# Kernel optimization log

Measured on AMD Instinct MI355X. Metric: run time of the kernel, lower is better.

## Reference

```python
import jax, jax.numpy as jnp
import numpy as np
from jax.scipy.special import gammaln

INTERVAL_STEPS = (1, -1, -3, 3, 4, -4)
MARGIN = 0.5


def _build_transition(S):
    # T[f, t, i] = 1 if t == f + interval_steps[i], else 0 (within support)
    T = np.zeros((S, S, len(INTERVAL_STEPS)), dtype=np.float32)
    for i, s in enumerate(INTERVAL_STEPS):
        if s > 0:
            f = np.arange(0, S - s)
        else:
            f = np.arange(-s, S)
        T[f, f + s, i] = 1.0
    return jnp.asarray(T)


def _forward(data, log_weights):
    n_data, C = data.shape
    S = int(np.ceil((2 * MARGIN + 1) * C))              # n_dist_support = 256
    center = int(np.round((MARGIN + 0.5) * C))           # reference_center = 128
    down = -min(min(INTERVAL_STEPS), 0)
    up = max(max(INTERVAL_STEPS), 0)
    n_iters = int(np.ceil(max(center / down, (S - center) / up))) + 1  # 33
    T = _build_transition(S)

    # Poisson-weighted Markov diffusion
    w = jnp.exp(log_weights)
    rate = w.sum(axis=1)                                 # [d]
    p = w / rate[:, None]                                # [d, i] interval step probs
    log_rate = jnp.log(rate)
    run0 = jnp.zeros((n_data, S), data.dtype).at[:, center].set(1.0)
    acc0 = jnp.zeros((n_data, S), data.dtype)

    def diff_step(carry, n):
        acc, run = carry
        step_prob = jnp.exp(n * log_rate - rate - gammaln(n + 1.0))  # Poisson pmf(n)
        acc = acc + step_prob[:, None] * run
        # einsum('fti,di,df->dt') done as two controlled contractions
        tmp = jnp.einsum('fti,df->dti', T, run)          # [d, t, i]
        run = jnp.einsum('dti,di->dt', tmp, p)           # [d, t]
        return (acc, run), None

    (acc, _), _ = jax.lax.scan(diff_step, (acc0, run0),
                               jnp.arange(n_iters, dtype=data.dtype))
    icd = acc / acc.sum(axis=1, keepdims=True)           # [d, S]

    # match distributions: min over shifts of DKL(data || normalized slice)
    n_shifts = S - C + 1
    pz = jnp.isclose(data, 0.0)
    safe_p = jnp.where(pz, 1.0, data)
    plogp = jnp.where(pz, 0.0, data * jnp.log(safe_p))   # [d, C]

    def match_step(carry, shift):
        best_loss, best_dist = carry
        d = jax.lax.dynamic_slice_in_dim(icd, shift, C, axis=1)
        d = d / d.sum(axis=1, keepdims=True)
        logq = jnp.log(jnp.maximum(d, 1e-38))            # guard fp32 underflow at edges
        loss = (plogp - jnp.where(pz, 0.0, data * logq)).sum(axis=1)
        cond = loss < best_loss
        return (jnp.where(cond, loss, best_loss),
                jnp.where(cond[:, None], d, best_dist)), None

    init = (jnp.full((n_data,), jnp.inf, data.dtype), jnp.zeros_like(data))
    (matched_loss, matched_dist), _ = jax.lax.scan(match_step, init, jnp.arange(n_shifts))
    return matched_loss


def setup_inputs() -> dict:
    key = jax.random.key(0)
    k1, k2 = jax.random.split(key)
    u = jax.random.uniform(k1, (4096, 128), jnp.float32)
    data = u / u.sum(axis=1, keepdims=True)              # rows are distributions
    # small weights -> Poisson rates ~6, so cum prob is allclose(1) before iter 33,
    # matching the original module's break-at-effective_min_iterations behavior
    log_weights = 0.1 * jax.random.normal(k2, (4096, 6), jnp.float32)
    return {"data": data, "log_weights": log_weights}


def reference(data, log_weights):
    return _forward(data, log_weights)
```

## Files before the change

kernel.cpp:

```cpp
#include <hip/hip_runtime.h>
#include <math.h>

#define NC      128
#define NSTATE  256
#define NITERS  33
#define NSTEPS  6
#define RPB     4
#define CL2     (-126.22347f)
#define LN2     (0.6931471805599453f)

__global__ __launch_bounds__(256)
void tonal_diffusion_kernel(const float* __restrict__ data,
                            const float* __restrict__ logw,
                            float* __restrict__ out, int n_rows)
{
    const int wid  = threadIdx.x >> 6;
    const int lane = threadIdx.x & 63;
    const int row  = blockIdx.x * RPB + wid;
    if (row >= n_rows) return;

    __shared__ float licd_s[RPB][NSTATE];
    __shared__ float P_s   [RPB][NSTATE];
    __shared__ float dsh_s [RPB][NC];
    float* __restrict__ licd = licd_s[wid];
    float* __restrict__ P    = P_s[wid];
    float* __restrict__ dsh  = dsh_s[wid];

    float rate, p0, p1, p2, p3, p4, p5;
    {
        const float* lw = logw + row * NSTEPS;
        p0 = expf(lw[0]); p1 = expf(lw[1]); p2 = expf(lw[2]);
        p3 = expf(lw[3]); p4 = expf(lw[4]); p5 = expf(lw[5]);
        rate = ((p0 + p1) + (p2 + p3)) + (p4 + p5);
        const float inv = 1.0f / rate;
        p0 *= inv; p1 *= inv; p2 *= inv; p3 *= inv; p4 *= inv; p5 *= inv;
    }

    float plogp;
    {
        const float2 dv = *(const float2*)(data + row * NC + 2 * lane);
        const float d0 = (dv.x > 1e-8f) ? dv.x : 0.f;
        const float d1 = (dv.y > 1e-8f) ? dv.y : 0.f;
        *(float2*)(dsh + 2 * lane) = make_float2(d0, d1);
        float pl = 0.f;
        if (d0 > 0.f) pl += d0 * logf(d0);
        if (d1 > 0.f) pl += d1 * logf(d1);
        #pragma unroll
        for (int off = 1; off < 64; off <<= 1) pl += __shfl_xor(pl, off, 64);
        plogp = pl;
    }

    float r0 = 0.f, r1 = 0.f, r2 = 0.f, r3 = 0.f;
    if (lane == 32) r0 = 1.0f;
    float a0 = 0.f, a1 = 0.f, a2 = 0.f, a3 = 0.f;
    float sp = expf(-rate);
    const float mL = (lane == 0)  ? 0.f : 1.f;
    const float mR = (lane == 63) ? 0.f : 1.f;
    #pragma unroll
    for (int n = 0; n < NITERS; ++n) {
        a0 += sp * r0; a1 += sp * r1; a2 += sp * r2; a3 += sp * r3;
        const float L0 = __shfl_up(r0, 1, 64) * mL;
        const float L1 = __shfl_up(r1, 1, 64) * mL;
        const float L2 = __shfl_up(r2, 1, 64) * mL;
        const float L3 = __shfl_up(r3, 1, 64) * mL;
        const float R0 = __shfl_down(r0, 1, 64) * mR;
        const float R1 = __shfl_down(r1, 1, 64) * mR;
        const float R2 = __shfl_down(r2, 1, 64) * mR;
        const float R3 = __shfl_down(r3, 1, 64) * mR;
        const float n0 = p0*L3 + p1*r1 + p2*r3 + p3*L1 + p4*L0 + p5*R0;
        const float n1 = p0*r0 + p1*r2 + p2*R0 + p3*L2 + p4*L1 + p5*R1;
        const float n2 = p0*r1 + p1*r3 + p2*R1 + p3*L3 + p4*L2 + p5*R2;
        const float n3 = p0*r2 + p1*R0 + p2*R2 + p3*r0 + p4*L3 + p5*R3;
        r0 = n0; r1 = n1; r2 = n2; r3 = n3;
        sp = sp * rate * (1.0f / (float)(n + 1));
    }

    *(float4*)(licd + 4 * lane) = make_float4(log2f(a0), log2f(a1), log2f(a2), log2f(a3));

    const float s0 = a0, s1 = s0 + a1, s2 = s1 + a2, s3 = s2 + a3;
    float t = s3;
    #pragma unroll
    for (int off = 1; off < 64; off <<= 1) {
        const float u = __shfl_up(t, off, 64);
        if (lane >= off) t += u;
    }
    const float base = t - s3;
    *(float4*)(P + 4 * lane) = make_float4(base + s0, base + s1, base + s2, base + s3);

    const int sA = lane, sB = lane + 64;
    const float zA = log2f(P[sA + 127] - (sA ? P[sA - 1] : 0.f));
    const float zB = log2f(P[sB + 127] - P[sB - 1]);
    float accA = 0.f, accB = 0.f;
    const float* lc = licd + lane;
    #pragma unroll 8
    for (int idx = 0; idx < 64; ++idx)
        accA += dsh[idx] * fmaxf(lc[idx] - zA, CL2);
    #pragma unroll 8
    for (int idx = 64; idx < 128; ++idx) {
        const float v = lc[idx];
        accA += dsh[idx]      * fmaxf(v - zA, CL2);
        accB += dsh[idx - 64] * fmaxf(v - zB, CL2);
    }
    #pragma unroll 8
    for (int idx = 128; idx < 192; ++idx)
        accB += dsh[idx - 64] * fmaxf(lc[idx] - zB, CL2);
    float best = fminf(plogp - LN2 * accA, plogp - LN2 * accB);

    {
        const float z = log2f(P[255] - P[127]);
        float part = dsh[2 * lane]     * fmaxf(licd[128 + 2 * lane] - z, CL2)
                   + dsh[2 * lane + 1] * fmaxf(licd[129 + 2 * lane] - z, CL2);
        #pragma unroll
        for (int off = 1; off < 64; off <<= 1) part += __shfl_xor(part, off, 64);
        best = fminf(best, plogp - LN2 * part);
    }

    #pragma unroll
    for (int off = 1; off < 64; off <<= 1) best = fminf(best, __shfl_xor(best, off, 64));
    if (lane == 0) out[row] = best;
}

extern "C" void kernel_launch(void* const* d_in, const int* in_sizes, int n_in,
                              void* d_out, int out_size, void* d_ws, size_t ws_size,
                              hipStream_t stream)
{
    const float* data = (const float*)d_in[0];
    const float* logw = (const float*)d_in[1];
    float* out = (float*)d_out;
    const int n_rows = in_sizes[0] / NC;
    const int blocks = (n_rows + RPB - 1) / RPB;
    tonal_diffusion_kernel<<<blocks, 256, 0, stream>>>(data, logw, out, n_rows);
}
```

Baseline: 77.79 us.

## Use DPP lane shifts and phase-replicated LDS layout for vectorized shift scan

Replaces ds_bpermute-based shuffles in the diffusion loop with DPP wave shift-by-one (bound_ctrl zero-fills edges, removing mask multiplies). Stores four phase-shifted copies of log-icd in LDS so each lane can read aligned float4 vectors in the shift-matching loop, and reads data from global memory with a wave-uniform row index (scalar loads) instead of staging it in LDS. It trades 4x LDS footprint for fewer LDS instructions and relies on DPP wave_shr/wave_shl being supported on this target. The near-zero clamp on data is also dropped in the accumulation loops.

Result: faster. 75.27 us (-3.2%).

```diff
diff --git a/kernel.cpp b/kernel.cpp
--- a/kernel.cpp
+++ b/kernel.cpp
@@ -9,6 +9,18 @@
 #define CL2     (-126.22347f)
 #define LN2     (0.6931471805599453f)
 
+#define DPP_WAVE_SHL1 0x130
+#define DPP_WAVE_SHR1 0x138
+
+__device__ __forceinline__ float dpp_shr1(float x) {
+    return __int_as_float(__builtin_amdgcn_update_dpp(
+        0, __float_as_int(x), DPP_WAVE_SHR1, 0xf, 0xf, true));
+}
+__device__ __forceinline__ float dpp_shl1(float x) {
+    return __int_as_float(__builtin_amdgcn_update_dpp(
+        0, __float_as_int(x), DPP_WAVE_SHL1, 0xf, 0xf, true));
+}
+
 __global__ __launch_bounds__(256)
 void tonal_diffusion_kernel(const float* __restrict__ data,
                             const float* __restrict__ logw,
@@ -18,17 +30,18 @@
     const int lane = threadIdx.x & 63;
     const int row  = blockIdx.x * RPB + wid;
     if (row >= n_rows) return;
+    const int urow = __builtin_amdgcn_readfirstlane(row);
 
-    __shared__ float licd_s[RPB][NSTATE];
-    __shared__ float P_s   [RPB][NSTATE];
-    __shared__ float dsh_s [RPB][NC];
-    float* __restrict__ licd = licd_s[wid];
-    float* __restrict__ P    = P_s[wid];
-    float* __restrict__ dsh  = dsh_s[wid];
+    __shared__ __align__(16) float licdR_s[RPB][4][NSTATE];
+    __shared__ __align__(16) float P_s    [RPB][NSTATE];
+    float (* __restrict__ licdR)[NSTATE] = licdR_s[wid];
+    float * __restrict__ P               = P_s[wid];
+
+    const float* __restrict__ drow = data + (size_t)urow * NC;
 
     float rate, p0, p1, p2, p3, p4, p5;
     {
-        const float* lw = logw + row * NSTEPS;
+        const float* lw = logw + urow * NSTEPS;
         p0 = expf(lw[0]); p1 = expf(lw[1]); p2 = expf(lw[2]);
         p3 = expf(lw[3]); p4 = expf(lw[4]); p5 = expf(lw[5]);
         rate = ((p0 + p1) + (p2 + p3)) + (p4 + p5);
@@ -36,15 +49,12 @@
         p0 *= inv; p1 *= inv; p2 *= inv; p3 *= inv; p4 *= inv; p5 *= inv;
     }
 
+    const float2 dl = *(const float2*)(drow + 2 * lane);
     float plogp;
     {
-        const float2 dv = *(const float2*)(data + row * NC + 2 * lane);
-        const float d0 = (dv.x > 1e-8f) ? dv.x : 0.f;
-        const float d1 = (dv.y > 1e-8f) ? dv.y : 0.f;
-        *(float2*)(dsh + 2 * lane) = make_float2(d0, d1);
         float pl = 0.f;
-        if (d0 > 0.f) pl += d0 * logf(d0);
-        if (d1 > 0.f) pl += d1 * logf(d1);
+        if (dl.x > 1e-8f) pl += dl.x * logf(dl.x);
+        if (dl.y > 1e-8f) pl += dl.y * logf(dl.y);
         #pragma unroll
         for (int off = 1; off < 64; off <<= 1) pl += __shfl_xor(pl, off, 64);
         plogp = pl;
@@ -54,19 +64,13 @@
     if (lane == 32) r0 = 1.0f;
     float a0 = 0.f, a1 = 0.f, a2 = 0.f, a3 = 0.f;
     float sp = expf(-rate);
-    const float mL = (lane == 0)  ? 0.f : 1.f;
-    const float mR = (lane == 63) ? 0.f : 1.f;
     #pragma unroll
     for (int n = 0; n < NITERS; ++n) {
         a0 += sp * r0; a1 += sp * r1; a2 += sp * r2; a3 += sp * r3;
-        const float L0 = __shfl_up(r0, 1, 64) * mL;
-        const float L1 = __shfl_up(r1, 1, 64) * mL;
-        const float L2 = __shfl_up(r2, 1, 64) * mL;
-        const float L3 = __shfl_up(r3, 1, 64) * mL;
-        const float R0 = __shfl_down(r0, 1, 64) * mR;
-        const float R1 = __shfl_down(r1, 1, 64) * mR;
-        const float R2 = __shfl_down(r2, 1, 64) * mR;
-        const float R3 = __shfl_down(r3, 1, 64) * mR;
+        const float L0 = dpp_shr1(r0), L1 = dpp_shr1(r1),
+                    L2 = dpp_shr1(r2), L3 = dpp_shr1(r3);
+        const float R0 = dpp_shl1(r0), R1 = dpp_shl1(r1),
+                    R2 = dpp_shl1(r2), R3 = dpp_shl1(r3);
         const float n0 = p0*L3 + p1*r1 + p2*r3 + p3*L1 + p4*L0 + p5*R0;
         const float n1 = p0*r0 + p1*r2 + p2*R0 + p3*L2 + p4*L1 + p5*R1;
         const float n2 = p0*r1 + p1*r3 + p2*R1 + p3*L3 + p4*L2 + p5*R2;
@@ -75,41 +79,69 @@
         sp = sp * rate * (1.0f / (float)(n + 1));
     }
 
-    *(float4*)(licd + 4 * lane) = make_float4(log2f(a0), log2f(a1), log2f(a2), log2f(a3));
+    {
+        const float l0 = log2f(a0), l1 = log2f(a1), l2 = log2f(a2), l3 = log2f(a3);
+        const float nl0 = dpp_shl1(l0), nl1 = dpp_shl1(l1), nl2 = dpp_shl1(l2);
+        *(float4*)&licdR[0][4 * lane] = make_float4(l0, l1, l2, l3);
+        *(float4*)&licdR[1][4 * lane] = make_float4(l1, l2, l3, nl0);
+        *(float4*)&licdR[2][4 * lane] = make_float4(l2, l3, nl0, nl1);
+        *(float4*)&licdR[3][4 * lane] = make_float4(l3, nl0, nl1, nl2);
+    }
 
-    const float s0 = a0, s1 = s0 + a1, s2 = s1 + a2, s3 = s2 + a3;
-    float t = s3;
-    #pragma unroll
-    for (int off = 1; off < 64; off <<= 1) {
-        const float u = __shfl_up(t, off, 64);
-        if (lane >= off) t += u;
+    {
+        const float s0 = a0, s1 = s0 + a1, s2 = s1 + a2, s3 = s2 + a3;
+        float t = s3;
+        #pragma unroll
+        for (int off = 1; off < 64; off <<= 1) {
+            const float u = __shfl_up(t, off, 64);
+            if (lane >= off) t += u;
+        }
+        const float base = t - s3;
+        *(float4*)&P[4 * lane] = make_float4(base + s0, base + s1, base + s2, base + s3);
     }
-    const float base = t - s3;
-    *(float4*)(P + 4 * lane) = make_float4(base + s0, base + s1, base + s2, base + s3);
 
-    const int sA = lane, sB = lane + 64;
-    const float zA = log2f(P[sA + 127] - (sA ? P[sA - 1] : 0.f));
-    const float zB = log2f(P[sB + 127] - P[sB - 1]);
+    const int phi = lane & 3;
+    const float* __restrict__ lcp = &licdR[phi][lane - phi];
+    const float zA = log2f(P[lane + 127] - (lane ? P[lane - 1] : 0.f));
+    const float zB = log2f(P[lane + 191] - P[lane + 63]);
     float accA = 0.f, accB = 0.f;
-    const float* lc = licd + lane;
     #pragma unroll 8
-    for (int idx = 0; idx < 64; ++idx)
-        accA += dsh[idx] * fmaxf(lc[idx] - zA, CL2);
-    #pragma unroll 8
-    for (int idx = 64; idx < 128; ++idx) {
-        const float v = lc[idx];
-        accA += dsh[idx]      * fmaxf(v - zA, CL2);
-        accB += dsh[idx - 64] * fmaxf(v - zB, CL2);
+    for (int m = 0; m < 16; ++m) {
+        const float4 v = *(const float4*)(lcp + 4 * m);
+        const int c = 4 * m;
+        accA += drow[c + 0] * fmaxf(v.x - zA, CL2);
+        accA += drow[c + 1] * fmaxf(v.y - zA, CL2);
+        accA += drow[c + 2] * fmaxf(v.z - zA, CL2);
+        accA += drow[c + 3] * fmaxf(v.w - zA, CL2);
     }
     #pragma unroll 8
-    for (int idx = 128; idx < 192; ++idx)
-        accB += dsh[idx - 64] * fmaxf(lc[idx] - zB, CL2);
+    for (int m = 16; m < 32; ++m) {
+        const float4 v = *(const float4*)(lcp + 4 * m);
+        const int c = 4 * m;
+        accA += drow[c + 0] * fmaxf(v.x - zA, CL2);
+        accA += drow[c + 1] * fmaxf(v.y - zA, CL2);
+        accA += drow[c + 2] * fmaxf(v.z - zA, CL2);
+        accA += drow[c + 3] * fmaxf(v.w - zA, CL2);
+        accB += drow[c - 64 + 0] * fmaxf(v.x - zB, CL2);
+        accB += drow[c - 64 + 1] * fmaxf(v.y - zB, CL2);
+        accB += drow[c - 64 + 2] * fmaxf(v.z - zB, CL2);
+        accB += drow[c - 64 + 3] * fmaxf(v.w - zB, CL2);
+    }
+    #pragma unroll 8
+    for (int m = 32; m < 48; ++m) {
+        const float4 v = *(const float4*)(lcp + 4 * m);
+        const int c = 4 * m - 64;
+        accB += drow[c + 0] * fmaxf(v.x - zB, CL2);
+        accB += drow[c + 1] * fmaxf(v.y - zB, CL2);
+        accB += drow[c + 2] * fmaxf(v.z - zB, CL2);
+        accB += drow[c + 3] * fmaxf(v.w - zB, CL2);
+    }
     float best = fminf(plogp - LN2 * accA, plogp - LN2 * accB);
 
     {
         const float z = log2f(P[255] - P[127]);
-        float part = dsh[2 * lane]     * fmaxf(licd[128 + 2 * lane] - z, CL2)
-                   + dsh[2 * lane + 1] * fmaxf(licd[129 + 2 * lane] - z, CL2);
+        const float2 lv = *(const float2*)(&licdR[0][128 + 2 * lane]);
+        float part = dl.x * fmaxf(lv.x - z, CL2) + dl.y * fmaxf(lv.y - z, CL2);
         #pragma unroll
         for (int off = 1; off < 64; off <<= 1) part += __shfl_xor(part, off, 64);
         best = fminf(best, plogp - LN2 * part);
```
